# Kernel tuning notes

Measured on AMD Instinct MI355X. Metric: run time of the kernel, lower is better.

Reference implementation:

```python
import jax, jax.numpy as jnp
import numpy as np

N = 50000      # nodes
E = 800000     # edges (before self-loops)
D = 128        # hid_d
H = 8          # heads
C = D // H     # per-head channels
L = 3          # layers
SLOPE = 0.2    # GATv2 leaky_relu negative slope
EPS = 1e-5     # LayerNorm eps


def setup_inputs() -> dict:
    key = jax.random.key(0)
    ks = jax.random.split(key, 8)
    x = jax.random.normal(ks[0], (N, D), dtype=jnp.float32)
    ei = jax.random.randint(ks[1], (2, E), 0, N, dtype=jnp.int32)
    s = 1.0 / np.sqrt(D)
    Wl = jax.random.normal(ks[2], (L, D, D), dtype=jnp.float32) * s   # source transform per layer
    Wr = jax.random.normal(ks[3], (L, D, D), dtype=jnp.float32) * s   # target transform per layer
    att = jax.random.normal(ks[4], (L, H, C), dtype=jnp.float32) * (1.0 / np.sqrt(C))
    bias = jnp.zeros((L, D), dtype=jnp.float32)
    gamma = jnp.ones((L, D), dtype=jnp.float32)
    beta = jnp.zeros((L, D), dtype=jnp.float32)
    return {"x": x, "Wl": Wl, "Wr": Wr, "att": att, "bias": bias,
            "gamma": gamma, "beta": beta, "ei": ei}


def _layernorm(y, g, b):
    mu = jnp.mean(y, axis=-1, keepdims=True)
    var = jnp.mean(jnp.square(y - mu), axis=-1, keepdims=True)
    return (y - mu) * jax.lax.rsqrt(var + EPS) * g + b


def reference(x, Wl, Wr, att, bias, gamma, beta, ei):
    # append self-loops (PyG GATv2Conv default add_self_loops=True)
    loops = jnp.arange(N, dtype=ei.dtype)
    src = jnp.concatenate([ei[0], loops])  # [E+N]
    dst = jnp.concatenate([ei[1], loops])  # [E+N]
    h = x
    for l in range(L):
        xl = (h @ Wl[l]).reshape(N, H, C)   # source-side features
        xr = (h @ Wr[l]).reshape(N, H, C)   # target-side features
        feat = xl[src] + xr[dst]            # [E+N, H, C] per-edge gather
        logits = jnp.einsum('ehc,hc->eh', jax.nn.leaky_relu(feat, SLOPE), att[l])
        # segment softmax over incoming edges of each dst node
        m = jax.ops.segment_max(logits, dst, num_segments=N)
        ex = jnp.exp(logits - m[dst])
        denom = jax.ops.segment_sum(ex, dst, num_segments=N)
        alpha = ex / denom[dst]             # [E+N, H]
        msg = alpha[:, :, None] * xl[src]   # [E+N, H, C]
        out = jax.ops.segment_sum(msg, dst, num_segments=N).reshape(N, H * C) + bias[l]
        # wrapper: h = h + dropout(elu(norm(gat(h)))) ; dropout = identity (eval)
        h = h + jax.nn.elu(_layernorm(out, gamma[l], beta[l]))
    return h
```

## Files before the change

kernel.cpp:

```cpp
#include <hip/hip_runtime.h>
#include <hip/hip_fp16.h>
#include <math.h>

#define N_NODES 50000
#define N_EDGES 800000
#define D 128
#define L 3
#define SLOPE 0.2f
#define LN_EPS 1e-5f
#define ETOT (N_EDGES + N_NODES)
#define SCAN_BLOCKS ((N_NODES + 1023) / 1024)

typedef _Float16 half8 __attribute__((ext_vector_type(8)));
typedef _Float16 h2v  __attribute__((ext_vector_type(2)));
typedef float f32x4 __attribute__((ext_vector_type(4)));


__global__ void rank_hist_kernel(const int* __restrict__ ei, int* __restrict__ counts,
                                 unsigned char* __restrict__ rank) {
    int idx = blockIdx.x * blockDim.x + threadIdx.x;
    if (idx >= ETOT) return;
    int d = (idx < N_EDGES) ? ei[N_EDGES + idx] : (idx - N_EDGES);
    rank[idx] = (unsigned char)atomicAdd(&counts[d], 1);
}

__global__ __launch_bounds__(1024) void scan1_kernel(const int* __restrict__ counts,
                                                     int* __restrict__ offsets,
                                                     int* __restrict__ bsum) {
    __shared__ int wsum[16];
    int tid = threadIdx.x;
    int lane = tid & 63, w = tid >> 6;
    int i = blockIdx.x * 1024 + tid;
    int v = (i < N_NODES) ? counts[i] : 0;
    int sc = v;
    #pragma unroll
    for (int off = 1; off < 64; off <<= 1) {
        int u = __shfl_up(sc, off);
        if (lane >= off) sc += u;
    }
    if (lane == 63) wsum[w] = sc;
    __syncthreads();
    if (w == 0) {
        int t2 = (lane < 16) ? wsum[lane] : 0;
        #pragma unroll
        for (int off = 1; off < 16; off <<= 1) {
            int u = __shfl_up(t2, off);
            if (lane >= off) t2 += u;
        }
        if (lane < 16) wsum[lane] = t2;
    }
    __syncthreads();
    int wpref = (w == 0) ? 0 : wsum[w - 1];
    if (i < N_NODES) offsets[i] = wpref + sc - v;
    if (tid == 0) bsum[blockIdx.x] = wsum[15];
}

__global__ __launch_bounds__(64) void scan2_kernel(const int* __restrict__ bsum,
                                                   int* __restrict__ bpre) {
    int lane = threadIdx.x;
    int v = (lane < SCAN_BLOCKS) ? bsum[lane] : 0;
    int sc = v;
    #pragma unroll
    for (int off = 1; off < 64; off <<= 1) {
        int u = __shfl_up(sc, off);
        if (lane >= off) sc += u;
    }
    if (lane < SCAN_BLOCKS) bpre[lane] = sc - v;
}

__global__ __launch_bounds__(1024) void scan3_kernel(int* __restrict__ offsets,
                                                     const int* __restrict__ bpre) {
    int i = blockIdx.x * 1024 + threadIdx.x;
    if (i < N_NODES) offsets[i] += bpre[blockIdx.x];
    if (i == 0) offsets[N_NODES] = ETOT;
}

__global__ void scatter_kernel(const int* __restrict__ ei, const int* __restrict__ offsets,
                               const unsigned char* __restrict__ rank,
                               unsigned short* __restrict__ sorted16) {
    int idx = blockIdx.x * blockDim.x + threadIdx.x;
    if (idx >= ETOT) return;
    int s, d;
    if (idx < N_EDGES) { s = ei[idx]; d = ei[N_EDGES + idx]; }
    else               { s = d = idx - N_EDGES; }
    sorted16[offsets[d] + rank[idx]] = (unsigned short)s;
}


__global__ __launch_bounds__(256) void wfrag_kernel(const float* __restrict__ Wl,
                                                    const float* __restrict__ Wr,
                                                    _Float16* __restrict__ Wfrag) {
    int u = blockIdx.x * 256 + threadIdx.x;
    if (u >= 3 * 4096) return;
    int lane = u & 63, nt = (u >> 6) & 7, kt = (u >> 9) & 3, y = (u >> 11) & 1, l = u >> 12;
    int r = lane & 15, q = lane >> 4;
    const float* W = (y ? Wr : Wl) + (size_t)l * D * D;
    half8 v;
    #pragma unroll
    for (int j = 0; j < 8; ++j)
        v[j] = (_Float16)W[(kt * 32 + q * 8 + j) * D + nt * 16 + r];
    *(half8*)&Wfrag[(size_t)u * 8] = v;
}


__global__ __launch_bounds__(256) void gemm_mfma_kernel(
        const float* __restrict__ h, const _Float16* __restrict__ WfragL,
        _Float16* __restrict__ xlh, _Float16* __restrict__ xrh) {
    __shared__ half8 Afrag[1024];
    int t = threadIdx.x;
    int row0 = blockIdx.x * 64;
    {
        int kt = t >> 6, q = (t >> 4) & 3, r = t & 15;
        int kc = kt * 4 + q;
        #pragma unroll
        for (int i = 0; i < 4; ++i) {
            int row = row0 + i * 16 + r;
            float4 f0 = make_float4(0.f, 0.f, 0.f, 0.f), f1 = f0;
            if (row < N_NODES) {
                const float* p = &h[(size_t)row * D + kc * 8];
                f0 = *(const float4*)p;
                f1 = *(const float4*)(p + 4);
            }
            half8 v;
            v[0] = (_Float16)f0.x; v[1] = (_Float16)f0.y;
            v[2] = (_Float16)f0.z; v[3] = (_Float16)f0.w;
            v[4] = (_Float16)f1.x; v[5] = (_Float16)f1.y;
            v[6] = (_Float16)f1.z; v[7] = (_Float16)f1.w;
            Afrag[i * 256 + t] = v;
        }
    }
    __syncthreads();
    int w = t >> 6, lane = t & 63;
    f32x4 acc[16];
    #pragma unroll
    for (int i = 0; i < 16; ++i) acc[i] = (f32x4){0.f, 0.f, 0.f, 0.f};
    #pragma unroll
    for (int kt = 0; kt < 4; ++kt) {
        half8 a = Afrag[(w * 4 + kt) * 64 + lane];
        #pragma unroll
        for (int y = 0; y < 2; ++y) {
            #pragma unroll
            for (int nt = 0; nt < 8; ++nt) {
                half8 b = *(const half8*)&WfragL[(size_t)(((y * 4 + kt) * 8 + nt) * 64 + lane) * 8];
                acc[y * 8 + nt] = __builtin_amdgcn_mfma_f32_16x16x32_f16(a, b, acc[y * 8 + nt], 0, 0, 0);
            }
        }
    }
    int rq = lane >> 4, rc = lane & 15;
    int rbase = row0 + w * 16 + rq * 4;
    #pragma unroll
    for (int y = 0; y < 2; ++y) {
        _Float16* out = y ? xrh : xlh;
        #pragma unroll
        for (int nt = 0; nt < 8; ++nt) {
            #pragma unroll
            for (int reg = 0; reg < 4; ++reg) {
                int row = rbase + reg;
                if (row < N_NODES)
                    out[(size_t)row * D + nt * 16 + rc] = (_Float16)acc[y * 8 + nt][reg];
            }
        }
    }
}


__device__ __forceinline__ float head_reduce8(float p) {
    int t;
    t = __builtin_amdgcn_update_dpp(0, __float_as_int(p), 0xB1, 0xF, 0xF, true);
    p += __int_as_float(t);
    t = __builtin_amdgcn_update_dpp(0, __float_as_int(p), 0x4E, 0xF, 0xF, true);
    p += __int_as_float(t);
    t = __builtin_amdgcn_update_dpp(0, __float_as_int(p), 0x141, 0xF, 0xF, true);
    p += __int_as_float(t);
    return p;
}

__device__ __forceinline__ float logit2(h2v v, h2v xrv2, h2v att2, h2v slope2) {
    h2v f  = v + xrv2;
    h2v lf = __builtin_elementwise_max(f, f * slope2);
    return __builtin_amdgcn_fdot2(lf, att2, 0.f, false);
}

__device__ __forceinline__ float2 h2f(h2v v) {
    return make_float2((float)v[0], (float)v[1]);
}

template<bool PRED>
__device__ __forceinline__ void edge_block16(
        const char* __restrict__ xlb, unsigned off, unsigned laneoff, int j, int cnt,
        h2v xrv2, h2v att2, h2v slope2,
        float& s, float& ax0, float& ay0, float& ax1, float& ay1) {
    unsigned oo[16];
    #pragma unroll
    for (int k = 0; k < 16; ++k)
        oo[k] = __builtin_amdgcn_readlane(off, j + k) + laneoff;
    h2v vv[16];
    #pragma unroll
    for (int k = 0; k < 16; ++k) vv[k] = *(const h2v*)(xlb + oo[k]);
    float pp[16];
    #pragma unroll
    for (int k = 0; k < 16; ++k) pp[k] = logit2(vv[k], xrv2, att2, slope2);
    #pragma unroll
    for (int k = 0; k < 16; ++k) pp[k] = head_reduce8(pp[k]);
    float ee[16];
    #pragma unroll
    for (int k = 0; k < 16; ++k) ee[k] = __builtin_amdgcn_exp2f(pp[k]);
    if (PRED) {
        #pragma unroll
        for (int k = 0; k < 16; ++k)
            if (j + k >= cnt) ee[k] = 0.f;
    }
    s += (((ee[0] + ee[1]) + (ee[2] + ee[3])) + ((ee[4] + ee[5]) + (ee[6] + ee[7])))
       + (((ee[8] + ee[9]) + (ee[10] + ee[11])) + ((ee[12] + ee[13]) + (ee[14] + ee[15])));
    #pragma unroll
    for (int k = 0; k < 16; k += 2) {
        float2 f0 = h2f(vv[k]), f1 = h2f(vv[k + 1]);
        ax0 = fmaf(ee[k], f0.x, ax0);     ay0 = fmaf(ee[k], f0.y, ay0);
        ax1 = fmaf(ee[k + 1], f1.x, ax1); ay1 = fmaf(ee[k + 1], f1.y, ay1);
    }
}

__global__ __launch_bounds__(256) void gat_node_kernel(
        const _Float16* __restrict__ xlh, const _Float16* __restrict__ xrh,
        const int* __restrict__ offsets, const unsigned short* __restrict__ sorted16,
        const float* __restrict__ att_l, const float* __restrict__ bias_l,
        const float* __restrict__ gamma_l, const float* __restrict__ beta_l,
        const float* __restrict__ hin, float* __restrict__ hout) {
    int node = (blockIdx.x * blockDim.x + threadIdx.x) >> 6;
    if (node >= N_NODES) return;
    int lane = threadIdx.x & 63;
    unsigned laneoff = lane * 4u;
    h2v xrv2 = ((const h2v*)xrh)[(size_t)node * 64 + lane];
    float2 attf = *(const float2*)&att_l[2 * lane];
    h2v att2;
    att2[0] = (_Float16)(attf.x * 1.44269504f);
    att2[1] = (_Float16)(attf.y * 1.44269504f);
    h2v slope2;
    slope2[0] = (_Float16)SLOPE;
    slope2[1] = (_Float16)SLOPE;
    int beg = offsets[node], end = offsets[node + 1];
    float s = 0.f, ax0 = 0.f, ay0 = 0.f, ax1 = 0.f, ay1 = 0.f;
    const char* xlb = (const char*)xlh;
    for (int c0 = beg; c0 < end; c0 += 64) {
        int cnt = end - c0; if (cnt > 64) cnt = 64;
        unsigned idx = sorted16[c0 + (lane < cnt ? lane : cnt - 1)];
        unsigned off = idx << 8;
        int j = 0;
        for (; j + 16 <= cnt; j += 16)
            edge_block16<false>(xlb, off, laneoff, j, cnt, xrv2, att2, slope2,
                                s, ax0, ay0, ax1, ay1);
        if (j < cnt)
            edge_block16<true>(xlb, off, laneoff, j, cnt, xrv2, att2, slope2,
                               s, ax0, ay0, ax1, ay1);
    }
    float accx = ax0 + ax1, accy = ay0 + ay1;
    float inv = 1.f / s;
    float2 bia = *(const float2*)&bias_l[2 * lane];
    float o0 = accx * inv + bia.x;
    float o1 = accy * inv + bia.y;
    float sum = o0 + o1, sq = o0 * o0 + o1 * o1;
    #pragma unroll
    for (int msk = 1; msk < 64; msk <<= 1) {
        sum += __shfl_xor(sum, msk);
        sq  += __shfl_xor(sq, msk);
    }
    float mu   = sum * (1.f / 128.f);
    float var  = sq * (1.f / 128.f) - mu * mu;
    float rstd = rsqrtf(var + LN_EPS);
    float2 gam = *(const float2*)&gamma_l[2 * lane];
    float2 bet = *(const float2*)&beta_l[2 * lane];
    float y0 = (o0 - mu) * rstd * gam.x + bet.x;
    float y1 = (o1 - mu) * rstd * gam.y + bet.y;
    y0 = y0 > 0.f ? y0 : __expf(y0) - 1.f;
    y1 = y1 > 0.f ? y1 : __expf(y1) - 1.f;
    size_t di = (size_t)node * D + 2 * lane;
    float2 hv = *(const float2*)&hin[di];
    hv.x += y0; hv.y += y1;
    *(float2*)&hout[di] = hv;
}


extern "C" void kernel_launch(void* const* d_in, const int* in_sizes, int n_in,
                              void* d_out, int out_size, void* d_ws, size_t ws_size,
                              hipStream_t stream) {
    const float* x     = (const float*)d_in[0];
    const float* Wl    = (const float*)d_in[1];
    const float* Wr    = (const float*)d_in[2];
    const float* att   = (const float*)d_in[3];
    const float* bias  = (const float*)d_in[4];
    const float* gamma = (const float*)d_in[5];
    const float* beta  = (const float*)d_in[6];
    const int*   ei    = (const int*)d_in[7];
    float* h = (float*)d_out;

    char* ws = (char*)d_ws;
    _Float16* xlh = (_Float16*)ws;   ws += (size_t)N_NODES * D * sizeof(_Float16);
    _Float16* xrh = (_Float16*)ws;   ws += (size_t)N_NODES * D * sizeof(_Float16);
    _Float16* Wfrag = (_Float16*)ws; ws += (size_t)3 * 4096 * 8 * sizeof(_Float16);
    int* offsets = (int*)ws;         ws += (size_t)(N_NODES + 4) * sizeof(int);
    int* counts  = (int*)ws;         ws += (size_t)N_NODES * sizeof(int);
    int* bsum    = (int*)ws;         ws += 64 * sizeof(int);
    int* bpre    = (int*)ws;         ws += 64 * sizeof(int);
    unsigned char* rank = (unsigned char*)ws;  ws += (size_t)ETOT;
    unsigned short* sorted16 = (unsigned short*)ws;

    wfrag_kernel<<<48, 256, 0, stream>>>(Wl, Wr, Wfrag);
    (void)hipMemsetAsync(counts, 0, (size_t)N_NODES * sizeof(int), stream);
    rank_hist_kernel<<<(ETOT + 255) / 256, 256, 0, stream>>>(ei, counts, rank);
    scan1_kernel<<<SCAN_BLOCKS, 1024, 0, stream>>>(counts, offsets, bsum);
    scan2_kernel<<<1, 64, 0, stream>>>(bsum, bpre);
    scan3_kernel<<<SCAN_BLOCKS, 1024, 0, stream>>>(offsets, bpre);
    scatter_kernel<<<(ETOT + 255) / 256, 256, 0, stream>>>(ei, offsets, rank, sorted16);

    for (int l = 0; l < L; ++l) {
        const float* hin = (l == 0) ? x : h;
        gemm_mfma_kernel<<<(N_NODES + 63) / 64, 256, 0, stream>>>(
            hin, Wfrag + (size_t)l * 4096 * 8, xlh, xrh);
        gat_node_kernel<<<(N_NODES * 64 + 255) / 256, 256, 0, stream>>>(
            xlh, xrh, offsets, sorted16,
            att + (size_t)l * D, bias + (size_t)l * D,
            gamma + (size_t)l * D, beta + (size_t)l * D, hin, h);
    }
}
```

Baseline: 371.3 us.

## Remap GAT aggregation to 8 edges per wave with 16-channel per-lane loads

The per-node aggregation now has each wave handle 8 edges at once, with each lane covering one head's 16 channels (two 16-byte loads) of one edge. Previously the wave walked edges one at a time, each lane loading 4 bytes. This replaces the per-edge readlane and head-reduction DPP chains with one bpermute per 8 edges and a single cross-edge reduction at the end. It also precomputes the log2e-scaled fp16 attention vector once in the wfrag kernel. The cost is 16 float accumulators per lane plus a final select tree, and partially wasted slots when the degree is not a multiple of 8.

```diff
diff --git a/kernel.cpp b/kernel.cpp
--- a/kernel.cpp
+++ b/kernel.cpp
@@ -89,8 +89,11 @@
 
 __global__ __launch_bounds__(256) void wfrag_kernel(const float* __restrict__ Wl,
                                                     const float* __restrict__ Wr,
-                                                    _Float16* __restrict__ Wfrag) {
+                                                    const float* __restrict__ att,
+                                                    _Float16* __restrict__ Wfrag,
+                                                    _Float16* __restrict__ att16) {
     int u = blockIdx.x * 256 + threadIdx.x;
+    if (u < 3 * D) att16[u] = (_Float16)(att[u] * 1.44269504f);
     if (u >= 3 * 4096) return;
     int lane = u & 63, nt = (u >> 6) & 7, kt = (u >> 9) & 3, y = (u >> 11) & 1, l = u >> 12;
     int r = lane & 15, q = lane >> 4;
@@ -164,7 +167,7 @@
 }
 
 
-__device__ __forceinline__ float head_reduce8(float p) {
+__device__ __forceinline__ float ereduce8(float p) {
     int t;
     t = __builtin_amdgcn_update_dpp(0, __float_as_int(p), 0xB1, 0xF, 0xF, true);
     p += __int_as_float(t);
@@ -175,89 +178,90 @@
     return p;
 }
 
-__device__ __forceinline__ float logit2(h2v v, h2v xrv2, h2v att2, h2v slope2) {
-    h2v f  = v + xrv2;
-    h2v lf = __builtin_elementwise_max(f, f * slope2);
-    return __builtin_amdgcn_fdot2(lf, att2, 0.f, false);
-}
-
-__device__ __forceinline__ float2 h2f(h2v v) {
-    return make_float2((float)v[0], (float)v[1]);
-}
-
-template<bool PRED>
-__device__ __forceinline__ void edge_block16(
-        const char* __restrict__ xlb, unsigned off, unsigned laneoff, int j, int cnt,
-        h2v xrv2, h2v att2, h2v slope2,
-        float& s, float& ax0, float& ay0, float& ax1, float& ay1) {
-    unsigned oo[16];
-    #pragma unroll
-    for (int k = 0; k < 16; ++k)
-        oo[k] = __builtin_amdgcn_readlane(off, j + k) + laneoff;
-    h2v vv[16];
-    #pragma unroll
-    for (int k = 0; k < 16; ++k) vv[k] = *(const h2v*)(xlb + oo[k]);
-    float pp[16];
-    #pragma unroll
-    for (int k = 0; k < 16; ++k) pp[k] = logit2(vv[k], xrv2, att2, slope2);
-    #pragma unroll
-    for (int k = 0; k < 16; ++k) pp[k] = head_reduce8(pp[k]);
-    float ee[16];
-    #pragma unroll
-    for (int k = 0; k < 16; ++k) ee[k] = __builtin_amdgcn_exp2f(pp[k]);
-    if (PRED) {
-        #pragma unroll
-        for (int k = 0; k < 16; ++k)
-            if (j + k >= cnt) ee[k] = 0.f;
-    }
-    s += (((ee[0] + ee[1]) + (ee[2] + ee[3])) + ((ee[4] + ee[5]) + (ee[6] + ee[7])))
-       + (((ee[8] + ee[9]) + (ee[10] + ee[11])) + ((ee[12] + ee[13]) + (ee[14] + ee[15])));
-    #pragma unroll
-    for (int k = 0; k < 16; k += 2) {
-        float2 f0 = h2f(vv[k]), f1 = h2f(vv[k + 1]);
-        ax0 = fmaf(ee[k], f0.x, ax0);     ay0 = fmaf(ee[k], f0.y, ay0);
-        ax1 = fmaf(ee[k + 1], f1.x, ax1); ay1 = fmaf(ee[k + 1], f1.y, ay1);
+__device__ __forceinline__ h2v pair_of(half8 v, int i) {
+    switch (i) {
+        case 0: return __builtin_shufflevector(v, v, 0, 1);
+        case 1: return __builtin_shufflevector(v, v, 2, 3);
+        case 2: return __builtin_shufflevector(v, v, 4, 5);
+        default: return __builtin_shufflevector(v, v, 6, 7);
     }
 }
 
 __global__ __launch_bounds__(256) void gat_node_kernel(
         const _Float16* __restrict__ xlh, const _Float16* __restrict__ xrh,
         const int* __restrict__ offsets, const unsigned short* __restrict__ sorted16,
-        const float* __restrict__ att_l, const float* __restrict__ bias_l,
+        const _Float16* __restrict__ att16, const float* __restrict__ bias_l,
         const float* __restrict__ gamma_l, const float* __restrict__ beta_l,
         const float* __restrict__ hin, float* __restrict__ hout) {
     int node = (blockIdx.x * blockDim.x + threadIdx.x) >> 6;
     if (node >= N_NODES) return;
     int lane = threadIdx.x & 63;
-    unsigned laneoff = lane * 4u;
-    h2v xrv2 = ((const h2v*)xrh)[(size_t)node * 64 + lane];
-    float2 attf = *(const float2*)&att_l[2 * lane];
-    h2v att2;
-    att2[0] = (_Float16)(attf.x * 1.44269504f);
-    att2[1] = (_Float16)(attf.y * 1.44269504f);
-    h2v slope2;
-    slope2[0] = (_Float16)SLOPE;
-    slope2[1] = (_Float16)SLOPE;
+    int e = lane & 7, h = lane >> 3;
+    unsigned hoff = (unsigned)h * 32u;
+    const char* xrb = (const char*)xrh + ((size_t)node << 8) + hoff;
+    half8 xr0 = *(const half8*)xrb;
+    half8 xr1 = *(const half8*)(xrb + 16);
+    const char* atb = (const char*)att16 + hoff;
+    half8 at0 = *(const half8*)atb;
+    half8 at1 = *(const half8*)(atb + 16);
+    h2v slope2; slope2[0] = (_Float16)SLOPE; slope2[1] = (_Float16)SLOPE;
     int beg = offsets[node], end = offsets[node + 1];
-    float s = 0.f, ax0 = 0.f, ay0 = 0.f, ax1 = 0.f, ay1 = 0.f;
+    float s = 0.f;
+    float acc[16];
+    #pragma unroll
+    for (int c = 0; c < 16; ++c) acc[c] = 0.f;
     const char* xlb = (const char*)xlh;
+    int e4 = e << 2;
     for (int c0 = beg; c0 < end; c0 += 64) {
         int cnt = end - c0; if (cnt > 64) cnt = 64;
-        unsigned idx = sorted16[c0 + (lane < cnt ? lane : cnt - 1)];
-        unsigned off = idx << 8;
-        int j = 0;
-        for (; j + 16 <= cnt; j += 16)
-            edge_block16<false>(xlb, off, laneoff, j, cnt, xrv2, att2, slope2,
-                                s, ax0, ay0, ax1, ay1);
-        if (j < cnt)
-            edge_block16<true>(xlb, off, laneoff, j, cnt, xrv2, att2, slope2,
-                               s, ax0, ay0, ax1, ay1);
-    }
-    float accx = ax0 + ax1, accy = ay0 + ay1;
+        unsigned idxoff = (unsigned)sorted16[c0 + (lane < cnt ? lane : cnt - 1)] << 8;
+        for (int j = 0; j < cnt; j += 8) {
+            int slot = j + e;
+            unsigned off = (unsigned)__builtin_amdgcn_ds_bpermute((j << 2) + e4, (int)idxoff);
+            const char* p = xlb + (off + hoff);
+            half8 v0 = *(const half8*)p;
+            half8 v1 = *(const half8*)(p + 16);
+            float pacc = 0.f;
+            #pragma unroll
+            for (int i = 0; i < 4; ++i) {
+                h2v f = pair_of(v0, i) + pair_of(xr0, i);
+                h2v lf = __builtin_elementwise_max(f, f * slope2);
+                pacc = __builtin_amdgcn_fdot2(lf, pair_of(at0, i), pacc, false);
+            }
+            #pragma unroll
+            for (int i = 0; i < 4; ++i) {
+                h2v f = pair_of(v1, i) + pair_of(xr1, i);
+                h2v lf = __builtin_elementwise_max(f, f * slope2);
+                pacc = __builtin_amdgcn_fdot2(lf, pair_of(at1, i), pacc, false);
+            }
+            float ev = (slot < cnt) ? __builtin_amdgcn_exp2f(pacc) : 0.f;
+            s += ev;
+            #pragma unroll
+            for (int i = 0; i < 4; ++i) {
+                h2v a = pair_of(v0, i), b = pair_of(v1, i);
+                acc[2 * i]     = fmaf(ev, (float)a[0], acc[2 * i]);
+                acc[2 * i + 1] = fmaf(ev, (float)a[1], acc[2 * i + 1]);
+                acc[8 + 2 * i]     = fmaf(ev, (float)b[0], acc[8 + 2 * i]);
+                acc[8 + 2 * i + 1] = fmaf(ev, (float)b[1], acc[8 + 2 * i + 1]);
+            }
+        }
+    }
+    s = ereduce8(s);
+    #pragma unroll
+    for (int c = 0; c < 16; ++c) acc[c] = ereduce8(acc[c]);
+    bool s2 = (e & 4) != 0, s1 = (e & 2) != 0, s0 = (e & 1) != 0;
+    float m[8];
+    #pragma unroll
+    for (int c = 0; c < 8; ++c) m[c] = s2 ? acc[c + 8] : acc[c];
+    float n[4];
+    #pragma unroll
+    for (int c = 0; c < 4; ++c) n[c] = s1 ? m[c + 4] : m[c];
+    float a0 = s0 ? n[2] : n[0];
+    float a1 = s0 ? n[3] : n[1];
     float inv = 1.f / s;
     float2 bia = *(const float2*)&bias_l[2 * lane];
-    float o0 = accx * inv + bia.x;
-    float o1 = accy * inv + bia.y;
+    float o0 = a0 * inv + bia.x;
+    float o1 = a1 * inv + bia.y;
     float sum = o0 + o1, sq = o0 * o0 + o1 * o1;
     #pragma unroll
     for (int msk = 1; msk < 64; msk <<= 1) {
@@ -297,6 +301,7 @@
     _Float16* xlh = (_Float16*)ws;   ws += (size_t)N_NODES * D * sizeof(_Float16);
     _Float16* xrh = (_Float16*)ws;   ws += (size_t)N_NODES * D * sizeof(_Float16);
     _Float16* Wfrag = (_Float16*)ws; ws += (size_t)3 * 4096 * 8 * sizeof(_Float16);
+    _Float16* att16 = (_Float16*)ws; ws += (size_t)3 * D * sizeof(_Float16);
     int* offsets = (int*)ws;         ws += (size_t)(N_NODES + 4) * sizeof(int);
     int* counts  = (int*)ws;         ws += (size_t)N_NODES * sizeof(int);
     int* bsum    = (int*)ws;         ws += 64 * sizeof(int);
@@ -304,7 +309,7 @@
     unsigned char* rank = (unsigned char*)ws;  ws += (size_t)ETOT;
     unsigned short* sorted16 = (unsigned short*)ws;
 
-    wfrag_kernel<<<48, 256, 0, stream>>>(Wl, Wr, Wfrag);
+    wfrag_kernel<<<48, 256, 0, stream>>>(Wl, Wr, att, Wfrag, att16);
     (void)hipMemsetAsync(counts, 0, (size_t)N_NODES * sizeof(int), stream);
     rank_hist_kernel<<<(ETOT + 255) / 256, 256, 0, stream>>>(ei, counts, rank);
     scan1_kernel<<<SCAN_BLOCKS, 1024, 0, stream>>>(counts, offsets, bsum);
@@ -318,7 +323,7 @@
             hin, Wfrag + (size_t)l * 4096 * 8, xlh, xrh);
         gat_node_kernel<<<(N_NODES * 64 + 255) / 256, 256, 0, stream>>>(
             xlh, xrh, offsets, sorted16,
-            att + (size_t)l * D, bias + (size_t)l * D,
+            att16 + (size_t)l * D, bias + (size_t)l * D,
             gamma + (size_t)l * D, beta + (size_t)l * D, hin, h);
     }
 }
```

After: 444.8 us. 19.8% more time.
